# Optimization experiments

Measured on AMD Instinct MI355X. Metric: run time of the kernel, lower is better.

## Reference

```python
import jax, jax.numpy as jnp
import numpy as np

jax.config.update("jax_enable_x64", True)  # hash math needs int64, matching torch .long()

IN_DIM = 3
N_LEVELS = 16
F = 2
B = 1.38
BASE = 16
T = 524309  # nextprime(2**19)
PS = np.array([1, 19349663, 83492791], dtype=np.int64)  # first in_dim primes
ENTRIES_NUM = np.array([[int(BASE * B ** i)] * IN_DIM for i in range(N_LEVELS)], dtype=np.int64)
ENTRIES_CNT = np.prod(ENTRIES_NUM, axis=1)
ENTRIES_SIZE = (1.0 / (ENTRIES_NUM - 1)).astype(np.float32)
ENTRIES_SUM = np.cumsum(ENTRIES_CNT)
S = int(np.argmax(ENTRIES_CNT > T))  # start_hash = 6
H = N_LEVELS - S                     # 10 hashed levels
K = 2 ** IN_DIM                      # 8 cube corners
DENSE_SIZE = int(ENTRIES_SUM[S - 1])  # 822944
# binary corner offsets, MSB-first (matches the source's bit loop)
OFFSETS = np.array([[(i >> (IN_DIM - 1 - d)) & 1 for d in range(IN_DIM)] for i in range(K)], dtype=np.float32)
# row-major strides for dense levels: prod of trailing resolutions per dim
STRIDES = np.stack([np.prod(ENTRIES_NUM[:S, i + 1:], axis=1) for i in range(IN_DIM)], axis=1)  # (S,3)
BASE_OFF = np.concatenate([np.zeros(1, np.int64), ENTRIES_SUM[:S - 1]])  # per-level offset into dense
BOUNDS = np.array([[0., 0., 0.], [1., 1., 1.]], dtype=np.float32)


def setup_inputs() -> dict:
    key = jax.random.key(0)
    k1, k2, k3 = jax.random.split(key, 3)
    xyz = jax.random.uniform(k1, (2, 65536, 3), dtype=jnp.float32)
    dense = (jax.random.uniform(k2, (DENSE_SIZE, F), dtype=jnp.float32) * 2 - 1) * 1e-4
    hash_table = (jax.random.uniform(k3, (H, T, F), dtype=jnp.float32) * 2 - 1) * 1e-4
    return {"xyz": xyz, "dense": dense, "hash_table": hash_table}


def _forward(xyz, dense, hash_table):
    bash = xyz.shape
    x = xyz.reshape(-1, IN_DIM)
    N = x.shape[0]
    x = (x - BOUNDS[0]) / (BOUNDS[1] - BOUNDS[0])  # normalize to [0,1]
    flt = x[None] / jnp.asarray(ENTRIES_SIZE)[:, None]  # (L,N,3): coords in grid units
    intx = (flt[:, :, None] + jnp.asarray(OFFSETS)[None, None]).astype(jnp.int64)  # (L,N,K,3)
    intx = jnp.clip(intx, 0, jnp.asarray(ENTRIES_NUM)[:, None, None] - 1)
    off = flt - intx[:, :, 0].astype(flt.dtype)  # (L,N,3) fractional offset from corner 0
    # dense (non-hashed) levels: row-major linear index + level base offset
    ind_dense = (intx[:S] * jnp.asarray(STRIDES)[:, None, None, :]).sum(-1)  # (S,N,K)
    ind_dense = ind_dense + jnp.asarray(BASE_OFF)[:, None, None]
    # hashed levels: XOR of prime-multiplied coords, seeded with ones (as in source)
    ih = jnp.ones_like(intx[S:, ..., 0])
    for i in range(IN_DIM):
        ih = ih ^ (intx[S:, ..., i] * int(PS[i]))
    ih = ih % T  # (H,N,K)
    val_dense = dense[ind_dense]  # (S,N,K,F) gather
    val_hash = jnp.take_along_axis(hash_table, ih.reshape(H, -1)[..., None], axis=1).reshape(H, N, K, F)
    val = jnp.concatenate([val_dense, val_hash], axis=0)  # (L,N,K,F)
    o = jnp.asarray(OFFSETS)[None, None]  # (1,1,K,3)
    w = 1 - o + (2 * o - 1.0) * off[:, :, None]  # (L,N,K,3) per-dim lerp weights
    w = w[..., 0] * w[..., 1]  # NOTE: source multiplies only dims 0 and 1 (replicated faithfully)
    val = (w[..., None] * val).sum(-2)  # (L,N,F)
    val = jnp.transpose(val, (1, 0, 2)).reshape(N, N_LEVELS * F)  # (N, 32)
    out = jnp.concatenate([x, val], axis=-1)  # include_input -> (N, 35)
    return out.reshape(*bash[:-1], out.shape[-1])


def reference(xyz, dense, hash_table):
    return _forward(xyz, dense, hash_table)
```

## Files before the change

### kernel.cpp

```cpp
#include <hip/hip_runtime.h>
#include <cstdint>


namespace {
constexpr int NLEV   = 16;
constexpr int SDENSE = 6;
constexpr uint64_t T_HASH = 524309ull;

__constant__ int c_res[NLEV] = {16,22,30,42,58,80,110,152,210,290,400,553,763,1053,1453,2005};
__constant__ float c_es[NLEV] = {
    (float)(1.0/15.0),  (float)(1.0/21.0),  (float)(1.0/29.0),  (float)(1.0/41.0),
    (float)(1.0/57.0),  (float)(1.0/79.0),  (float)(1.0/109.0), (float)(1.0/151.0),
    (float)(1.0/209.0), (float)(1.0/289.0), (float)(1.0/399.0), (float)(1.0/552.0),
    (float)(1.0/762.0), (float)(1.0/1052.0),(float)(1.0/1452.0),(float)(1.0/2004.0)
};
__constant__ int c_base[SDENSE] = {0, 4096, 14744, 41744, 115832, 310944};
}

__device__ __forceinline__ void level_eval(
    const float* __restrict__ xyz,
    const float2* __restrict__ dense,
    const float2* __restrict__ hashtab,
    int n, int l, float& acc0, float& acc1,
    float& x0, float& x1, float& x2)
{
    x0 = xyz[3*n + 0];
    x1 = xyz[3*n + 1];
    x2 = xyz[3*n + 2];

    int   res = c_res[l];
    float es  = c_es[l];
    float f0 = x0 / es;
    float f1 = x1 / es;
    float f2 = x2 / es;
    int nm1 = res - 1;

    int i00 = min(max((int)f0, 0), nm1);
    int i01 = min(max((int)f1, 0), nm1);
    int i02 = min(max((int)f2, 0), nm1);
    int i10 = min(max((int)(f0 + 1.0f), 0), nm1);
    int i11 = min(max((int)(f1 + 1.0f), 0), nm1);
    int i12 = min(max((int)(f2 + 1.0f), 0), nm1);

    float off0 = f0 - (float)i00;
    float off1 = f1 - (float)i01;
    float w0a = 1.0f - off0, w0b = off0;
    float w1a = 1.0f - off1, w1b = off1;

    acc0 = 0.0f; acc1 = 0.0f;

    if (l < SDENSE) {
        int s0   = res * res;
        int base = c_base[l];
        int A0 = i00 * s0,  A1 = i10 * s0;
        int B0 = i01 * res, B1 = i11 * res;
        #pragma unroll
        for (int k = 0; k < 8; ++k) {
            int idx = ((k & 4) ? A1 : A0) + ((k & 2) ? B1 : B0)
                    + ((k & 1) ? i12 : i02) + base;
            float2 v = dense[idx];
            float w = ((k & 4) ? w0b : w0a) * ((k & 2) ? w1b : w1a);
            acc0 += w * v.x;
            acc1 += w * v.y;
        }
    } else {
        uint64_t a0 = (uint64_t)(uint32_t)i00;
        uint64_t a1 = (uint64_t)(uint32_t)i10;
        uint64_t b0 = (uint64_t)(uint32_t)i01 * 19349663ull;
        uint64_t b1 = (uint64_t)(uint32_t)i11 * 19349663ull;
        uint64_t c0 = (uint64_t)(uint32_t)i02 * 83492791ull;
        uint64_t c1 = (uint64_t)(uint32_t)i12 * 83492791ull;
        uint32_t rowbase = (uint32_t)(l - SDENSE) * (uint32_t)T_HASH;
        #pragma unroll
        for (int k = 0; k < 8; ++k) {
            uint64_t h = 1ull ^ ((k & 4) ? a1 : a0)
                              ^ ((k & 2) ? b1 : b0)
                              ^ ((k & 1) ? c1 : c0);
            uint32_t idx = rowbase + (uint32_t)(h % T_HASH);
            float2 v = hashtab[idx];
            float w = ((k & 4) ? w0b : w0a) * ((k & 2) ? w1b : w1a);
            acc0 += w * v.x;
            acc1 += w * v.y;
        }
    }
}

__global__ __launch_bounds__(256) void hashgrid_level(
    const float*  __restrict__ xyz,
    const float2* __restrict__ dense,
    const float2* __restrict__ hashtab,
    float2*       __restrict__ ws,
    int npts)
{
    int b = blockIdx.x;
    int x = b & 7;
    int s = b >> 3;
    int level, chunk;
    if (s < 640) {
        int g = 640 * x + s;
        level = 6 + (g >> 9);
        chunk = g & 511;
    } else {
        int h = 384 * (7 - x) + (s - 640);
        level = h >> 9;
        chunk = h & 511;
    }
    int n = (chunk << 8) + threadIdx.x;
    if (n >= npts) return;

    float acc0, acc1, x0, x1, x2;
    level_eval(xyz, dense, hashtab, n, level, acc0, acc1, x0, x1, x2);
    ws[(size_t)level * npts + n] = make_float2(acc0, acc1);
}

__global__ __launch_bounds__(256) void gather_out(
    const float*  __restrict__ xyz,
    const float2* __restrict__ ws,
    float*        __restrict__ out,
    int npts)
{
    int n = blockIdx.x * 256 + threadIdx.x;
    if (n >= npts) return;
    float* o = out + (size_t)n * 35;
    o[0] = xyz[3*n + 0];
    o[1] = xyz[3*n + 1];
    o[2] = xyz[3*n + 2];
    #pragma unroll
    for (int l = 0; l < NLEV; ++l) {
        float2 v = ws[(size_t)l * npts + n];
        o[3 + 2*l] = v.x;
        o[4 + 2*l] = v.y;
    }
}

__global__ __launch_bounds__(256) void hashgrid_mono(
    const float*  __restrict__ xyz,
    const float2* __restrict__ dense,
    const float2* __restrict__ hashtab,
    float*        __restrict__ out,
    int npts)
{
    int tid = blockIdx.x * 256 + threadIdx.x;
    int l = tid & (NLEV - 1);
    int n = tid >> 4;
    if (n >= npts) return;

    float acc0, acc1, x0, x1, x2;
    level_eval(xyz, dense, hashtab, n, l, acc0, acc1, x0, x1, x2);

    float* o = out + (size_t)n * 35;
    if (l == 0) { o[0] = x0; o[1] = x1; o[2] = x2; }
    o[3 + 2*l] = acc0;
    o[4 + 2*l] = acc1;
}

extern "C" void kernel_launch(void* const* d_in, const int* in_sizes, int n_in,
                              void* d_out, int out_size, void* d_ws, size_t ws_size,
                              hipStream_t stream) {
    const float*  xyz     = (const float*)d_in[0];
    const float2* dense   = (const float2*)d_in[1];
    const float2* hashtab = (const float2*)d_in[2];
    float* out = (float*)d_out;

    int npts = in_sizes[0] / 3;
    size_t ws_need = (size_t)NLEV * (size_t)npts * sizeof(float2);

    if (npts == 131072 && ws_size >= ws_need) {
        float2* ws = (float2*)d_ws;
        hashgrid_level<<<8192, 256, 0, stream>>>(xyz, dense, hashtab, ws, npts);
        gather_out<<<(npts + 255) / 256, 256, 0, stream>>>(xyz, ws, out, npts);
    } else {
        int total  = npts * NLEV;
        int blocks = (total + 255) / 256;
        hashgrid_mono<<<blocks, 256, 0, stream>>>(xyz, dense, hashtab, out, npts);
    }
}
```

Baseline: 174.0 us.

## Exploit z-weight collapse, vectorize dense loads, stage xyz and output via LDS

The reference drops the z weight, so the two z-corners share a weight. The kernel now sums each z-pair before weighting: dense levels fetch both corners with one 16-byte load, and hashed levels compute two hashes per xy corner. It also stages xyz in shared memory for coalesced loads, uses nontemporal stores and loads for the workspace, and changes the level/chunk-to-block mapping. The gather kernel builds each 35-float output row in LDS and writes it out as coalesced 16-byte stores. The risks are the unaligned 16-byte reads, the boundary select logic, and the removed bounds checks, which now assume npts is a multiple of 256.

```diff
diff --git a/kernel.cpp b/kernel.cpp
--- a/kernel.cpp
+++ b/kernel.cpp
@@ -6,6 +6,11 @@
 constexpr int NLEV   = 16;
 constexpr int SDENSE = 6;
 constexpr uint64_t T_HASH = 524309ull;
+
+typedef float f2v __attribute__((ext_vector_type(2)));
+typedef float f4v __attribute__((ext_vector_type(4)));
+struct __attribute__((packed, aligned(8))) F4A8 { f4v v; };
+static_assert(sizeof(F4A8) == 16, "");
 
 __constant__ int c_res[NLEV] = {16,22,30,42,58,80,110,152,210,290,400,553,763,1053,1453,2005};
 __constant__ float c_es[NLEV] = {
@@ -18,16 +23,11 @@
 }
 
 __device__ __forceinline__ void level_eval(
-    const float* __restrict__ xyz,
     const float2* __restrict__ dense,
     const float2* __restrict__ hashtab,
-    int n, int l, float& acc0, float& acc1,
-    float& x0, float& x1, float& x2)
-{
-    x0 = xyz[3*n + 0];
-    x1 = xyz[3*n + 1];
-    x2 = xyz[3*n + 2];
-
+    float x0, float x1, float x2, int l,
+    float& acc0, float& acc1)
+{
     int   res = c_res[l];
     float es  = c_es[l];
     float f0 = x0 / es;
@@ -41,11 +41,13 @@
     int i10 = min(max((int)(f0 + 1.0f), 0), nm1);
     int i11 = min(max((int)(f1 + 1.0f), 0), nm1);
     int i12 = min(max((int)(f2 + 1.0f), 0), nm1);
+    (void)i12;
 
     float off0 = f0 - (float)i00;
     float off1 = f1 - (float)i01;
     float w0a = 1.0f - off0, w0b = off0;
     float w1a = 1.0f - off1, w1b = off1;
+    float wxy0 = w0a * w1a, wxy1 = w0a * w1b, wxy2 = w0b * w1a, wxy3 = w0b * w1b;
 
     acc0 = 0.0f; acc1 = 0.0f;
 
@@ -54,33 +56,36 @@
         int base = c_base[l];
         int A0 = i00 * s0,  A1 = i10 * s0;
         int B0 = i01 * res, B1 = i11 * res;
+        int  zlo    = min(i02, nm1 - 1);
+        bool lowSel = (i02 == zlo);
         #pragma unroll
-        for (int k = 0; k < 8; ++k) {
-            int idx = ((k & 4) ? A1 : A0) + ((k & 2) ? B1 : B0)
-                    + ((k & 1) ? i12 : i02) + base;
-            float2 v = dense[idx];
-            float w = ((k & 4) ? w0b : w0a) * ((k & 2) ? w1b : w1a);
-            acc0 += w * v.x;
-            acc1 += w * v.y;
+        for (int k = 0; k < 4; ++k) {
+            int idx = ((k & 2) ? A1 : A0) + ((k & 1) ? B1 : B0) + zlo + base;
+            f4v v = reinterpret_cast<const F4A8*>(dense + idx)->v;
+            float lo0 = lowSel ? v.x : v.z;
+            float lo1 = lowSel ? v.y : v.w;
+            float w = (k & 2) ? ((k & 1) ? wxy3 : wxy2) : ((k & 1) ? wxy1 : wxy0);
+            acc0 += w * (lo0 + v.z);
+            acc1 += w * (lo1 + v.w);
         }
     } else {
         uint64_t a0 = (uint64_t)(uint32_t)i00;
         uint64_t a1 = (uint64_t)(uint32_t)i10;
         uint64_t b0 = (uint64_t)(uint32_t)i01 * 19349663ull;
         uint64_t b1 = (uint64_t)(uint32_t)i11 * 19349663ull;
-        uint64_t c0 = (uint64_t)(uint32_t)i02 * 83492791ull;
-        uint64_t c1 = (uint64_t)(uint32_t)i12 * 83492791ull;
+        uint64_t cz0 = (uint64_t)(uint32_t)i02 * 83492791ull;
+        uint64_t cz1 = (uint64_t)(uint32_t)min(i02 + 1, nm1) * 83492791ull;
         uint32_t rowbase = (uint32_t)(l - SDENSE) * (uint32_t)T_HASH;
         #pragma unroll
-        for (int k = 0; k < 8; ++k) {
-            uint64_t h = 1ull ^ ((k & 4) ? a1 : a0)
-                              ^ ((k & 2) ? b1 : b0)
-                              ^ ((k & 1) ? c1 : c0);
-            uint32_t idx = rowbase + (uint32_t)(h % T_HASH);
-            float2 v = hashtab[idx];
-            float w = ((k & 4) ? w0b : w0a) * ((k & 2) ? w1b : w1a);
-            acc0 += w * v.x;
-            acc1 += w * v.y;
+        for (int k = 0; k < 4; ++k) {
+            uint64_t hb = 1ull ^ ((k & 2) ? a1 : a0) ^ ((k & 1) ? b1 : b0);
+            uint32_t idx0 = rowbase + (uint32_t)((hb ^ cz0) % T_HASH);
+            uint32_t idx1 = rowbase + (uint32_t)((hb ^ cz1) % T_HASH);
+            float2 v0 = hashtab[idx0];
+            float2 v1 = hashtab[idx1];
+            float w = (k & 2) ? ((k & 1) ? wxy3 : wxy2) : ((k & 1) ? wxy1 : wxy0);
+            acc0 += w * (v0.x + v1.x);
+            acc1 += w * (v0.y + v1.y);
         }
     }
 }
@@ -96,21 +101,30 @@
     int x = b & 7;
     int s = b >> 3;
     int level, chunk;
-    if (s < 640) {
-        int g = 640 * x + s;
-        level = 6 + (g >> 9);
+    if (s < 768) {
+        int g = 768 * x + s;
+        level = 4 + (g >> 9);
         chunk = g & 511;
     } else {
-        int h = 384 * (7 - x) + (s - 640);
+        int h = 256 * x + (s - 768);
         level = h >> 9;
         chunk = h & 511;
     }
-    int n = (chunk << 8) + threadIdx.x;
-    if (n >= npts) return;
-
-    float acc0, acc1, x0, x1, x2;
-    level_eval(xyz, dense, hashtab, n, level, acc0, acc1, x0, x1, x2);
-    ws[(size_t)level * npts + n] = make_float2(acc0, acc1);
+    int n0 = chunk << 8;
+    int t  = threadIdx.x;
+
+    __shared__ float sxyz[768];
+    sxyz[t      ] = xyz[3 * n0 + t      ];
+    sxyz[t + 256] = xyz[3 * n0 + t + 256];
+    sxyz[t + 512] = xyz[3 * n0 + t + 512];
+    __syncthreads();
+    float x0 = sxyz[3 * t], x1 = sxyz[3 * t + 1], x2 = sxyz[3 * t + 2];
+
+    float acc0, acc1;
+    level_eval(dense, hashtab, x0, x1, x2, level, acc0, acc1);
+
+    f2v val = {acc0, acc1};
+    __builtin_nontemporal_store(val, (f2v*)(ws + (size_t)level * npts + n0 + t));
 }
 
 __global__ __launch_bounds__(256) void gather_out(
@@ -119,17 +133,32 @@
     float*        __restrict__ out,
     int npts)
 {
-    int n = blockIdx.x * 256 + threadIdx.x;
-    if (n >= npts) return;
-    float* o = out + (size_t)n * 35;
-    o[0] = xyz[3*n + 0];
-    o[1] = xyz[3*n + 1];
-    o[2] = xyz[3*n + 2];
+    __shared__ __align__(16) float tile[256 * 35];
+    int t  = threadIdx.x;
+    int n0 = blockIdx.x << 8;
+    int n  = n0 + t;
+
+    #pragma unroll
+    for (int j = 0; j < 3; ++j) {
+        int pos = t + (j << 8);
+        float v = xyz[3 * n0 + pos];
+        int pt = pos / 3, dim = pos - 3 * pt;
+        tile[pt * 35 + dim] = v;
+    }
     #pragma unroll
     for (int l = 0; l < NLEV; ++l) {
-        float2 v = ws[(size_t)l * npts + n];
-        o[3 + 2*l] = v.x;
-        o[4 + 2*l] = v.y;
+        f2v v = __builtin_nontemporal_load((const f2v*)(ws + (size_t)l * npts + n));
+        tile[t * 35 + 3 + 2 * l] = v.x;
+        tile[t * 35 + 4 + 2 * l] = v.y;
+    }
+    __syncthreads();
+
+    const f4v* src = (const f4v*)tile;
+    f4v* dst = (f4v*)(out + (size_t)n0 * 35);
+    #pragma unroll
+    for (int i = 0; i < 9; ++i) {
+        int idx = t + (i << 8);
+        if (idx < 2240) __builtin_nontemporal_store(src[idx], dst + idx);
     }
 }
 
@@ -145,8 +174,9 @@
     int n = tid >> 4;
     if (n >= npts) return;
 
-    float acc0, acc1, x0, x1, x2;
-    level_eval(xyz, dense, hashtab, n, l, acc0, acc1, x0, x1, x2);
+    float x0 = xyz[3*n+0], x1 = xyz[3*n+1], x2 = xyz[3*n+2];
+    float acc0, acc1;
+    level_eval(dense, hashtab, x0, x1, x2, l, acc0, acc1);
 
     float* o = out + (size_t)n * 35;
     if (l == 0) { o[0] = x0; o[1] = x1; o[2] = x2; }
@@ -168,7 +198,7 @@
     if (npts == 131072 && ws_size >= ws_need) {
         float2* ws = (float2*)d_ws;
         hashgrid_level<<<8192, 256, 0, stream>>>(xyz, dense, hashtab, ws, npts);
-        gather_out<<<(npts + 255) / 256, 256, 0, stream>>>(xyz, ws, out, npts);
+        gather_out<<<npts / 256, 256, 0, stream>>>(xyz, ws, out, npts);
     } else {
         int total  = npts * NLEV;
         int blocks = (total + 255) / 256;
```

Result: faster. 155.4 us (-10.7%).
